# Kernel optimization log

Measured on AMD Instinct MI355X. Metric: run time of the kernel, lower is better.

The kernel has to match this reference:

```python
import jax, jax.numpy as jnp
import numpy as np
from jax import lax

B_, L_, D_MODEL = 2, 1024, 1024
D_STATE, RANK, EXPAND, HEADDIM = 64, 4, 2, 64
D_INNER = EXPAND * D_MODEL
NHEADS = D_INNER // HEADDIM          # 32, divisible by RANK
KCONV = 4
DFF = 4 * D_MODEL
D_PROJ = 2 * D_INNER + 2 * RANK * D_STATE + NHEADS
EPS = 1e-6


def setup_inputs() -> dict:
    key = jax.random.key(0)
    ks = iter(jax.random.split(key, 40))
    def nrm(shape, scale=0.02):
        return jax.random.normal(next(ks), shape, jnp.float32) * scale
    inp = {
        "x": jax.random.normal(next(ks), (B_, L_, D_MODEL), jnp.float32),
        "mask": jnp.ones((B_, L_), jnp.bool_),
        "norm1_w": jnp.ones((D_MODEL,), jnp.float32),
        "norm2_w": jnp.ones((D_MODEL,), jnp.float32),
        "gate_w": nrm((D_MODEL, 2 * D_MODEL)),
        "outp_w": nrm((D_MODEL, D_MODEL)),
        "ffn_w1": nrm((DFF, D_MODEL)),
        "ffn_w3": nrm((DFF, D_MODEL)),
        "ffn_w2": nrm((D_MODEL, DFF)),
    }
    for p in ("f", "b"):
        inp[p + "_in_w"] = nrm((D_PROJ, D_MODEL))
        inp[p + "_conv_w"] = nrm((D_INNER, KCONV), 0.2)
        inp[p + "_conv_b"] = jnp.zeros((D_INNER,), jnp.float32)
        inp[p + "_dt_bias"] = nrm((NHEADS,), 0.5)
        inp[p + "_A_log"] = jnp.log(jnp.linspace(1.0, 16.0, NHEADS)).astype(jnp.float32)
        inp[p + "_D"] = jnp.ones((NHEADS,), jnp.float32)
        inp[p + "_out_w"] = nrm((D_MODEL, D_INNER))
    return inp


def rmsnorm(x, w):
    return x * lax.rsqrt(jnp.mean(x * x, axis=-1, keepdims=True) + EPS) * w


def flip_by_mask(x, mask):
    # reverse valid positions along seq dim, keep padding at end
    L = x.shape[1]
    lengths = mask.astype(jnp.int32).sum(axis=1)          # (B,)
    ar = jnp.arange(L, dtype=jnp.int32)[None, :]
    rev = jnp.clip(lengths[:, None] - 1 - ar, 0, L - 1)   # (B,L)
    out = jnp.take_along_axis(x, rev[..., None], axis=1)
    return out * mask[..., None].astype(x.dtype)


def dwconv_causal(x, w, b):
    # x: (B,L,C), w: (C,K) depthwise, causal
    k = w.shape[-1]
    xp = jnp.pad(x, ((0, 0), (k - 1, 0), (0, 0)))
    kern = w.T[:, None, :]                                # (K,1,C) WIO
    y = lax.conv_general_dilated(xp, kern, (1,), 'VALID',
                                 dimension_numbers=('NWC', 'WIO', 'NWC'),
                                 feature_group_count=x.shape[-1])
    return y + b


def ssd_scan(a, Bh, Ch, dt, x4):
    # a,dt:(B,L,H)  Bh,Ch:(B,L,H,N)  x4:(B,L,H,P)
    def step(S, t):
        a_t, B_t, C_t, dt_t, x_t = t
        S = a_t[..., None, None] * S + (dt_t[..., None] * B_t)[..., None] * x_t[..., None, :]
        y = jnp.einsum('bhn,bhnp->bhp', C_t, S)
        return S, y
    S0 = jnp.zeros((a.shape[0], a.shape[2], Bh.shape[-1], x4.shape[-1]), x4.dtype)
    seq = tuple(jnp.moveaxis(t, 1, 0) for t in (a, Bh, Ch, dt, x4))
    _, ys = lax.scan(step, S0, seq)
    return jnp.moveaxis(ys, 0, 1)                          # (B,L,H,P)


def mamba3(h, maskf, in_w, conv_w, conv_b, dt_bias, A_log, D):
    B, L, _ = h.shape
    proj = h @ in_w.T                                      # (B,L,D_PROJ)
    s0, s1, s2, s3 = D_INNER, 2 * D_INNER, 2 * D_INNER + RANK * D_STATE, 2 * D_INNER + 2 * RANK * D_STATE
    z, xs, Bm, Cm, dt = (proj[..., :s0], proj[..., s0:s1], proj[..., s1:s2],
                          proj[..., s2:s3], proj[..., s3:])
    xs = jax.nn.silu(dwconv_causal(xs * maskf[..., None], conv_w, conv_b)) * maskf[..., None]
    dt = jax.nn.softplus(dt + dt_bias) * maskf[..., None]  # (B,L,H)
    A = -jnp.exp(A_log)                                    # (H,)
    a = jnp.exp(dt * A)
    g = NHEADS // RANK
    Bh = jnp.repeat(Bm.reshape(B, L, RANK, D_STATE), g, axis=2)  # (B,L,H,N)
    Ch = jnp.repeat(Cm.reshape(B, L, RANK, D_STATE), g, axis=2)
    x4 = xs.reshape(B, L, NHEADS, HEADDIM)
    y = ssd_scan(a, Bh, Ch, dt, x4) + D[None, None, :, None] * x4
    return y.reshape(B, L, D_INNER) * jax.nn.silu(z)


def reference(x, mask, norm1_w,
              f_in_w, f_conv_w, f_conv_b, f_dt_bias, f_A_log, f_D, f_out_w,
              b_in_w, b_conv_w, b_conv_b, b_dt_bias, b_A_log, b_D, b_out_w,
              gate_w, outp_w, norm2_w, ffn_w1, ffn_w3, ffn_w2):
    maskf = mask.astype(x.dtype)
    h = rmsnorm(x, norm1_w)
    y_f = mamba3(h, maskf, f_in_w, f_conv_w, f_conv_b, f_dt_bias, f_A_log, f_D) @ f_out_w.T
    h_rev = flip_by_mask(h, mask)
    y_b = mamba3(h_rev, maskf, b_in_w, b_conv_w, b_conv_b, b_dt_bias, b_A_log, b_D) @ b_out_w.T
    y_b = flip_by_mask(y_b, mask)
    gate = jax.nn.sigmoid(jnp.concatenate([y_f, y_b], axis=-1) @ gate_w.T)
    x = x + (gate * y_f + (1.0 - gate) * y_b) @ outp_w.T
    h2 = rmsnorm(x, norm2_w)
    x = x + (jax.nn.silu(h2 @ ffn_w1.T) * (h2 @ ffn_w3.T)) @ ffn_w2.T
    return x * maskf[..., None]
```

## Files before the change

### kernel.cpp

```cpp
#include <hip/hip_runtime.h>


#define T_TOK  2048
#define LSEQ   1024
#define DMODEL 1024
#define DINNER 2048
#define DPROJ  4640
#define NHEADS 32
#define DFF    4096
#define QCH    64
#define NCH    16
#define SST    72

using f32x4  = __attribute__((ext_vector_type(4))) float;
using bf16x8 = __attribute__((ext_vector_type(8))) short;

typedef __attribute__((address_space(1))) const void* gas1;
typedef __attribute__((address_space(3))) void* las3;

__device__ __forceinline__ void gld16(const void* g, void* l) {
  __builtin_amdgcn_global_load_lds((gas1)g, (las3)l, 16, 0, 0);
}

#define VMWAIT8() asm volatile("s_waitcnt vmcnt(8)" ::: "memory")
#define VMWAIT4() asm volatile("s_waitcnt vmcnt(4)" ::: "memory")
#define VMWAIT0() asm volatile("s_waitcnt vmcnt(0)" ::: "memory")
#define SCHEDB()  __builtin_amdgcn_sched_barrier(0)
#define BARRIER() __builtin_amdgcn_s_barrier()

__device__ __forceinline__ unsigned short f2bf(float x) {
  unsigned int u = __float_as_uint(x);
  u = (u + 0x7FFFu + ((u >> 16) & 1u)) >> 16;
  return (unsigned short)u;
}
__device__ __forceinline__ float bf2f(unsigned short u) {
  return __uint_as_float((unsigned int)u << 16);
}
__device__ __forceinline__ float siluf_(float x) { return x / (1.f + expf(-x)); }

__device__ __forceinline__ uint4 pack8(const float4& a, const float4& b) {
  uint4 o;
  o.x = (unsigned)f2bf(a.x) | ((unsigned)f2bf(a.y) << 16);
  o.y = (unsigned)f2bf(a.z) | ((unsigned)f2bf(a.w) << 16);
  o.z = (unsigned)f2bf(b.x) | ((unsigned)f2bf(b.y) << 16);
  o.w = (unsigned)f2bf(b.z) | ((unsigned)f2bf(b.w) << 16);
  return o;
}

__device__ __forceinline__ void tile_decode(int& tm, int& tn) {
  const int gx = gridDim.x;
  int flat = blockIdx.y * gx + blockIdx.x;
  int nwg = gx * gridDim.y;
  int cpx = nwg >> 3;
  int swz = (flat & 7) * cpx + (flat >> 3);
  int width = gx << 4;
  int group = swz / width;
  int rem = swz - group * width;
  tm = (group << 4) + (rem & 15);
  tn = rem >> 4;
}

__global__ __launch_bounds__(256) void k_cvt(const float* __restrict__ s,
                                             unsigned short* __restrict__ d, int n) {
  int i = (blockIdx.x * 256 + threadIdx.x) * 4;
  if (i >= n) return;
  float4 v = *(const float4*)(s + i);
  ushort4 o;
  o.x = f2bf(v.x); o.y = f2bf(v.y); o.z = f2bf(v.z); o.w = f2bf(v.w);
  *(ushort4*)(d + i) = o;
}

__global__ __launch_bounds__(256) void k_cvt13(const float* __restrict__ f1,
                                               const float* __restrict__ f3,
                                               unsigned short* __restrict__ d) {
  int i = (blockIdx.x * 256 + threadIdx.x) * 4;
  int R = i >> 10, k = i & 1023;
  const float* src = (R & 1) ? f3 : f1;
  float4 v = *(const float4*)(src + (size_t)(R >> 1) * 1024 + k);
  ushort4 o;
  o.x = f2bf(v.x); o.y = f2bf(v.y); o.z = f2bf(v.z); o.w = f2bf(v.w);
  *(ushort4*)(d + i) = o;
}

__global__ __launch_bounds__(256) void k_rms1(const float* __restrict__ x,
                                              const float* __restrict__ w,
                                              unsigned short* __restrict__ h,
                                              unsigned short* __restrict__ hrev) {
  int row = blockIdx.x;
  int tid = threadIdx.x;
  const float4* xr = (const float4*)(x + (size_t)row * DMODEL);
  float4 v = xr[tid];
  float s = v.x * v.x + v.y * v.y + v.z * v.z + v.w * v.w;
  #pragma unroll
  for (int off = 32; off >= 1; off >>= 1) s += __shfl_down(s, off);
  __shared__ float red[4];
  int lane = tid & 63, wv = tid >> 6;
  if (lane == 0) red[wv] = s;
  __syncthreads();
  float tot = red[0] + red[1] + red[2] + red[3];
  float scale = rsqrtf(tot * (1.0f / 1024.0f) + 1e-6f);
  float4 w4 = ((const float4*)w)[tid];
  ushort4 o;
  o.x = f2bf(v.x * scale * w4.x);
  o.y = f2bf(v.y * scale * w4.y);
  o.z = f2bf(v.z * scale * w4.z);
  o.w = f2bf(v.w * scale * w4.w);
  ((ushort4*)(h + (size_t)row * DMODEL))[tid] = o;
  ((ushort4*)(hrev + (size_t)(row ^ 1023) * DMODEL))[tid] = o;
}

template<int EPI>
__global__ __launch_bounds__(256, 2)
void k_gemmT(const unsigned short* __restrict__ A0, const unsigned short* __restrict__ B0,
             void* __restrict__ C0v,
             const unsigned short* __restrict__ A1, const unsigned short* __restrict__ B1,
             void* __restrict__ C1v, int N, int K, int ldc) {
  __shared__ unsigned short lA0[128 * 64], lB0[128 * 64];
  __shared__ unsigned short lA1[128 * 64], lB1[128 * 64];
  const unsigned short* A = blockIdx.z ? A1 : A0;
  const unsigned short* B = blockIdx.z ? B1 : B0;
  void* Cv = blockIdx.z ? C1v : C0v;

  int tm, tn;
  tile_decode(tm, tn);

  const int tid  = threadIdx.x;
  const int lane = tid & 63;
  const int wave = tid >> 6;
  const int wm = (wave >> 1) * 64, wn = (wave & 1) * 64;
  const int fr = lane & 15, kh = lane >> 4;
  const int sr = lane >> 3;
  const int sc = ((lane & 7) ^ sr) * 8;

  f32x4 acc[4][4];
  #pragma unroll
  for (int m = 0; m < 4; ++m)
    #pragma unroll
    for (int n = 0; n < 4; ++n)
      acc[m][n] = f32x4{0.f, 0.f, 0.f, 0.f};

  auto stage = [&](unsigned short* dA, unsigned short* dB, int kt) {
    #pragma unroll
    for (int i = 0; i < 4; ++i) {
      int r = wave * 32 + i * 8 + sr;
      size_t arow = (size_t)(tm * 128 + r);
      int brow = tn * 128 + r; if (brow > N - 1) brow = N - 1;
      gld16(A + arow * K + kt + sc, dA + (wave * 32 + i * 8) * 64);
      gld16(B + (size_t)brow * K + kt + sc, dB + (wave * 32 + i * 8) * 64);
    }
  };
  auto compute = [&](const unsigned short* sA, const unsigned short* sB) {
    #pragma unroll
    for (int kk = 0; kk < 2; ++kk) {
      bf16x8 af[4], bfv[4];
      #pragma unroll
      for (int m = 0; m < 4; ++m) {
        int row = wm + m * 16 + fr;
        af[m] = *(const bf16x8*)&sA[row * 64 + (((kk * 4 + kh) ^ (row & 7)) * 8)];
      }
      #pragma unroll
      for (int n = 0; n < 4; ++n) {
        int row = wn + n * 16 + fr;
        bfv[n] = *(const bf16x8*)&sB[row * 64 + (((kk * 4 + kh) ^ (row & 7)) * 8)];
      }
      #pragma unroll
      for (int m = 0; m < 4; ++m)
        #pragma unroll
        for (int n = 0; n < 4; ++n)
          acc[m][n] = __builtin_amdgcn_mfma_f32_16x16x32_bf16(af[m], bfv[n], acc[m][n], 0, 0, 0);
    }
  };

  const int nt = K >> 6;
  stage(lA0, lB0, 0);
  for (int t = 0; t < nt; t += 2) {
    if (t + 1 < nt) { stage(lA1, lB1, (t + 1) << 6); VMWAIT8(); } else VMWAIT0();
    SCHEDB(); BARRIER(); SCHEDB();
    compute(lA0, lB0);
    BARRIER(); SCHEDB();
    if (t + 1 < nt) {
      if (t + 2 < nt) { stage(lA0, lB0, (t + 2) << 6); VMWAIT8(); } else VMWAIT0();
      SCHEDB(); BARRIER(); SCHEDB();
      compute(lA1, lB1);
      BARRIER(); SCHEDB();
    }
  }

  #pragma unroll
  for (int m = 0; m < 4; ++m) {
    int grow0 = tm * 128 + wm + m * 16 + kh * 4;
    #pragma unroll
    for (int n = 0; n < 4; ++n) {
      int gcol = tn * 128 + wn + n * 16 + fr;
      if (gcol >= N) continue;
      #pragma unroll
      for (int j = 0; j < 4; ++j) {
        int row = grow0 + j;
        float val = acc[m][n][j];
        if constexpr (EPI == 0) {
          ((float*)Cv)[(size_t)row * ldc + gcol] = val;
        } else {
          float other = __shfl_xor(val, 1);
          if (!(fr & 1))
            ((unsigned short*)Cv)[(size_t)row * DFF + (gcol >> 1)] = f2bf(siluf_(val) * other);
        }
      }
    }
  }
}

template<int EPI>
__global__ __launch_bounds__(256, 4)
void k_gemm64T(const unsigned short* __restrict__ A0, const unsigned short* __restrict__ B0,
               void* __restrict__ C0v,
               const unsigned short* __restrict__ A1, const unsigned short* __restrict__ B1,
               void* __restrict__ C1v, int N, int K, int ldc) {
  __shared__ unsigned short lA0[64 * 64], lB0[64 * 64];
  __shared__ unsigned short lA1[64 * 64], lB1[64 * 64];
  const unsigned short* A = blockIdx.z ? A1 : A0;
  const unsigned short* B = blockIdx.z ? B1 : B0;
  void* Cv = blockIdx.z ? C1v : C0v;

  int tm, tn;
  tile_decode(tm, tn);

  const int tid  = threadIdx.x;
  const int lane = tid & 63;
  const int wave = tid >> 6;
  const int wm = (wave >> 1) * 32, wn = (wave & 1) * 32;
  const int fr = lane & 15, kh = lane >> 4;
  const int sr = lane >> 3;
  const int sc = ((lane & 7) ^ sr) * 8;

  f32x4 acc[2][2];
  #pragma unroll
  for (int m = 0; m < 2; ++m)
    #pragma unroll
    for (int n = 0; n < 2; ++n)
      acc[m][n] = f32x4{0.f, 0.f, 0.f, 0.f};

  auto stage = [&](unsigned short* dA, unsigned short* dB, int kt) {
    #pragma unroll
    for (int i = 0; i < 2; ++i) {
      int r = wave * 16 + i * 8 + sr;
      size_t arow = (size_t)(tm * 64 + r);
      size_t brow = (size_t)(tn * 64 + r);
      gld16(A + arow * K + kt + sc, dA + (wave * 16 + i * 8) * 64);
      gld16(B + brow * K + kt + sc, dB + (wave * 16 + i * 8) * 64);
    }
  };
  auto compute = [&](const unsigned short* sA, const unsigned short* sB) {
    #pragma unroll
    for (int kk = 0; kk < 2; ++kk) {
      bf16x8 af[2], bfv[2];
      #pragma unroll
      for (int m = 0; m < 2; ++m) {
        int row = wm + m * 16 + fr;
        af[m] = *(const bf16x8*)&sA[row * 64 + (((kk * 4 + kh) ^ (row & 7)) * 8)];
      }
      #pragma unroll
      for (int n = 0; n < 2; ++n) {
        int row = wn + n * 16 + fr;
        bfv[n] = *(const bf16x8*)&sB[row * 64 + (((kk * 4 + kh) ^ (row & 7)) * 8)];
      }
      #pragma unroll
      for (int m = 0; m < 2; ++m)
        #pragma unroll
        for (int n = 0; n < 2; ++n)
          acc[m][n] = __builtin_amdgcn_mfma_f32_16x16x32_bf16(af[m], bfv[n], acc[m][n], 0, 0, 0);
    }
  };

  const int nt = K >> 6;
  stage(lA0, lB0, 0);
  for (int t = 0; t < nt; t += 2) {
    if (t + 1 < nt) { stage(lA1, lB1, (t + 1) << 6); VMWAIT4(); } else VMWAIT0();
    SCHEDB(); BARRIER(); SCHEDB();
    compute(lA0, lB0);
    BARRIER(); SCHEDB();
    if (t + 1 < nt) {
      if (t + 2 < nt) { stage(lA0, lB0, (t + 2) << 6); VMWAIT4(); } else VMWAIT0();
      SCHEDB(); BARRIER(); SCHEDB();
      compute(lA1, lB1);
      BARRIER(); SCHEDB();
    }
  }

  #pragma unroll
  for (int m = 0; m < 2; ++m) {
    int grow0 = tm * 64 + wm + m * 16 + kh * 4;
    #pragma unroll
    for (int n = 0; n < 2; ++n) {
      int gcol = tn * 64 + wn + n * 16 + fr;
      #pragma unroll
      for (int j = 0; j < 4; ++j) {
        int row = grow0 + j;
        float val = acc[m][n][j];
        if constexpr (EPI == 0) {
          ((float*)Cv)[(size_t)row * ldc + gcol] = val;
        } else if constexpr (EPI == 1) {
          unsigned short* yc = (unsigned short*)Cv;
          if (blockIdx.z == 0)
            yc[(size_t)row * DINNER + gcol] = f2bf(val);
          else
            yc[(size_t)(row ^ 1023) * DINNER + 1024 + gcol] = f2bf(val);
        } else if constexpr (EPI == 3) {
          float* o = (float*)Cv + (size_t)row * ldc + gcol;
          *o += val;
        } else {
          const unsigned short* yc = (const unsigned short*)C1v;
          float gv = 1.f / (1.f + expf(-val));
          float yf = bf2f(yc[(size_t)row * DINNER + gcol]);
          float yb = bf2f(yc[(size_t)row * DINNER + 1024 + gcol]);
          ((unsigned short*)Cv)[(size_t)row * 1024 + gcol] = f2bf(gv * yf + (1.f - gv) * yb);
        }
      }
    }
  }
}

__global__ __launch_bounds__(256) void k_prep(
    const float* __restrict__ proj, const float* __restrict__ convw,
    const float* __restrict__ convb, const float* __restrict__ dtb,
    const float* __restrict__ Alog,
    float* __restrict__ xs, float* __restrict__ dts, float* __restrict__ las_) {
  int row = blockIdx.x;
  int t = row & 1023;
  int tid = threadIdx.x;
  int c0 = tid * 8;
  float acc[8];
  #pragma unroll
  for (int j = 0; j < 8; ++j) acc[j] = convb[c0 + j];
  #pragma unroll
  for (int tap = 0; tap < 4; ++tap) {
    int tt = t - 3 + tap;
    if (tt < 0) continue;
    const float* src = proj + (size_t)(row - 3 + tap) * DPROJ + 2048 + c0;
    #pragma unroll
    for (int j = 0; j < 8; ++j)
      acc[j] = fmaf(src[j], convw[(c0 + j) * 4 + tap], acc[j]);
  }
  float* dst = xs + (size_t)row * DINNER + c0;
  #pragma unroll
  for (int j = 0; j < 8; ++j) dst[j] = siluf_(acc[j]);

  if (tid < 32) {
    float d = proj[(size_t)row * DPROJ + 4608 + tid] + dtb[tid];
    d = fmaxf(d, 0.f) + log1pf(expf(-fabsf(d)));
    dts[row * 32 + tid] = d;
    las_[row * 32 + tid] = -expf(Alog[tid]) * d;
  }
}

__global__ __launch_bounds__(256) void k_scan1(
    const float* __restrict__ projF, const float* __restrict__ projB,
    const float* __restrict__ xsF, const float* __restrict__ xsB,
    const float* __restrict__ dtF, const float* __restrict__ dtB_,
    const float* __restrict__ laF, const float* __restrict__ laB,
    float* __restrict__ Ssum, float* __restrict__ Pk) {
  const int dir = blockIdx.y;
  const float* proj = dir ? projB : projF;
  const float* xs   = dir ? xsB  : xsF;
  const float* dts  = dir ? dtB_ : dtF;
  const float* las  = dir ? laB  : laF;
  const int job = blockIdx.x;
  const int k = job & 15, h = (job >> 4) & 31, b = job >> 9;
  const int rg = h >> 3;
  const int jid = (dir * 64 + b * 32 + h) * NCH + k;
  const int tid = threadIdx.x;
  const int lane = tid & 63, wave = tid >> 6;
  const int fr = lane & 15, kh = lane >> 4;
  const size_t rb = (size_t)b * LSEQ + k * QCH;

  __shared__ __align__(16) unsigned short sBt[64 * SST];
  __shared__ __align__(16) unsigned short sXw[64 * SST];
  __shared__ float sDt[64], sLa[64], sW[64];

  if (tid < 64) {
    sDt[tid] = dts[(rb + tid) * 32 + h];
    sLa[tid] = las[(rb + tid) * 32 + h];
  }
  __syncthreads();
  if (wave == 0) {
    float v = sLa[lane];
    #pragma unroll
    for (int o = 1; o < 64; o <<= 1) {
      float u = __shfl_up(v, o);
      if (lane >= o) v += u;
    }
    float tot = __shfl(v, 63);
    sW[lane] = sDt[lane] * expf(tot - v);
    if (lane == 0) Pk[jid] = expf(tot);
  }
  __syncthreads();

  {
    int t = tid >> 2, c0 = (tid & 3) * 16;
    float wt = sW[t];
    const float* pB = proj + (rb + t) * DPROJ + 4096 + rg * 64 + c0;
    const float* pX = xs + (rb + t) * DINNER + h * 64 + c0;
    #pragma unroll
    for (int q = 0; q < 4; ++q) {
      float4 bv = *(const float4*)(pB + 4 * q);
      float4 xv = *(const float4*)(pX + 4 * q);
      int c = c0 + 4 * q;
      sBt[(c + 0) * SST + t] = f2bf(bv.x);
      sBt[(c + 1) * SST + t] = f2bf(bv.y);
      sBt[(c + 2) * SST + t] = f2bf(bv.z);
      sBt[(c + 3) * SST + t] = f2bf(bv.w);
      sXw[(c + 0) * SST + t] = f2bf(xv.x * wt);
      sXw[(c + 1) * SST + t] = f2bf(xv.y * wt);
      sXw[(c + 2) * SST + t] = f2bf(xv.z * wt);
      sXw[(c + 3) * SST + t] = f2bf(xv.w * wt);
    }
  }
  __syncthreads();

  f32x4 acc[4];
  #pragma unroll
  for (int n = 0; n < 4; ++n) acc[n] = f32x4{0.f, 0.f, 0.f, 0.f};
  #pragma unroll
  for (int kk = 0; kk < 2; ++kk) {
    int kc = kk * 4 + kh;
    bf16x8 a = *(const bf16x8*)&sXw[(wave * 16 + fr) * SST + kc * 8];
    #pragma unroll
    for (int n = 0; n < 4; ++n) {
      bf16x8 bb = *(const bf16x8*)&sBt[(n * 16 + fr) * SST + kc * 8];
      acc[n] = __builtin_amdgcn_mfma_f32_16x16x32_bf16(a, bb, acc[n], 0, 0, 0);
    }
  }
  float* dst = Ssum + (size_t)jid * 4096;
  #pragma unroll
  for (int n = 0; n < 4; ++n)
    #pragma unroll
    for (int j = 0; j < 4; ++j)
      dst[(wave * 16 + kh * 4 + j) * 64 + n * 16 + fr] = acc[n][j];
}

__global__ __launch_bounds__(256) void k_scan2(float* __restrict__ Sbuf,
                                               const float* __restrict__ Pk) {
  int e = blockIdx.x * 256 + threadIdx.x;
  int dbh = e >> 12, pn = e & 4095;
  float s = 0.f;
  #pragma unroll
  for (int k = 0; k < NCH; ++k) {
    size_t idx = (size_t)(dbh * NCH + k) * 4096 + pn;
    float loc = Sbuf[idx];
    Sbuf[idx] = s;
    s = Pk[dbh * NCH + k] * s + loc;
  }
}

__global__ __launch_bounds__(256) void k_scan3(
    const float* __restrict__ projF, const float* __restrict__ projB,
    const float* __restrict__ xsF, const float* __restrict__ xsB,
    const float* __restrict__ dtF, const float* __restrict__ dtB_,
    const float* __restrict__ laF, const float* __restrict__ laB,
    const float* __restrict__ DF, const float* __restrict__ DB,
    const float* __restrict__ Sstart,
    unsigned short* __restrict__ yzF, unsigned short* __restrict__ yzB) {
  const int dir = blockIdx.y;
  const float* proj = dir ? projB : projF;
  const float* xs   = dir ? xsB  : xsF;
  const float* dts  = dir ? dtB_ : dtF;
  const float* las  = dir ? laB  : laF;
  const float* Dv   = dir ? DB   : DF;
  unsigned short* yzout = dir ? yzB : yzF;

  const int job = blockIdx.x;
  const int k = job & 15, h = (job >> 4) & 31, b = job >> 9;
  const int rg = h >> 3;
  const int jid = (dir * 64 + b * 32 + h) * NCH + k;
  const int tid = threadIdx.x;
  const int lane = tid & 63, wave = tid >> 6;
  const int fr = lane & 15, kh = lane >> 4;
  const float Dh = Dv[h];
  const size_t rb = (size_t)b * LSEQ + k * QCH;

  __shared__ __align__(16) unsigned short sCm[64 * SST];
  __shared__ __align__(16) unsigned short sBm[64 * SST];
  __shared__ __align__(16) unsigned short sXt[64 * SST];
  __shared__ __align__(16) unsigned short sS0[64 * SST];
  __shared__ __align__(16) unsigned short sMm[64 * SST];
  __shared__ float sDt[64], sLa[64], sLc[64];

  if (tid < 64) {
    sDt[tid] = dts[(rb + tid) * 32 + h];
    sLa[tid] = las[(rb + tid) * 32 + h];
  }
  {
    int t = tid >> 2, c0 = (tid & 3) * 16;
    const float* pB = proj + (rb + t) * DPROJ + 4096 + rg * 64 + c0;
    const float* pC = proj + (rb + t) * DPROJ + 4352 + rg * 64 + c0;
    const float* pX = xs + (rb + t) * DINNER + h * 64 + c0;
    const float* pS = Sstart + (size_t)jid * 4096 + t * 64 + c0;
    float4 b0 = *(const float4*)(pB + 0),  b1 = *(const float4*)(pB + 4);
    float4 b2 = *(const float4*)(pB + 8),  b3 = *(const float4*)(pB + 12);
    float4 c0v = *(const float4*)(pC + 0), c1v = *(const float4*)(pC + 4);
    float4 c2v = *(const float4*)(pC + 8), c3v = *(const float4*)(pC + 12);
    float4 s0v = *(const float4*)(pS + 0), s1v = *(const float4*)(pS + 4);
    float4 s2v = *(const float4*)(pS + 8), s3v = *(const float4*)(pS + 12);
    *(uint4*)&sBm[t * SST + c0]     = pack8(b0, b1);
    *(uint4*)&sBm[t * SST + c0 + 8] = pack8(b2, b3);
    *(uint4*)&sCm[t * SST + c0]     = pack8(c0v, c1v);
    *(uint4*)&sCm[t * SST + c0 + 8] = pack8(c2v, c3v);
    *(uint4*)&sS0[t * SST + c0]     = pack8(s0v, s1v);
    *(uint4*)&sS0[t * SST + c0 + 8] = pack8(s2v, s3v);
    #pragma unroll
    for (int q = 0; q < 4; ++q) {
      float4 xv = *(const float4*)(pX + 4 * q);
      int c = c0 + 4 * q;
      sXt[(c + 0) * SST + t] = f2bf(xv.x);
      sXt[(c + 1) * SST + t] = f2bf(xv.y);
      sXt[(c + 2) * SST + t] = f2bf(xv.z);
      sXt[(c + 3) * SST + t] = f2bf(xv.w);
    }
  }
  __syncthreads();
  if (wave == 0) {
    float v = sLa[lane];
    #pragma unroll
    for (int o = 1; o < 64; o <<= 1) {
      float u = __shfl_up(v, o);
      if (lane >= o) v += u;
    }
    sLc[lane] = v;
  }
  __syncthreads();

  f32x4 g[4];
  #pragma unroll
  for (int n = 0; n < 4; ++n) g[n] = f32x4{0.f, 0.f, 0.f, 0.f};
  #pragma unroll
  for (int kk = 0; kk < 2; ++kk) {
    int kc = kk * 4 + kh;
    bf16x8 a = *(const bf16x8*)&sCm[(wave * 16 + fr) * SST + kc * 8];
    #pragma unroll
    for (int n = 0; n < 4; ++n) {
      bf16x8 bb = *(const bf16x8*)&sBm[(n * 16 + fr) * SST + kc * 8];
      g[n] = __builtin_amdgcn_mfma_f32_16x16x32_bf16(a, bb, g[n], 0, 0, 0);
    }
  }
  int t0 = wave * 16 + kh * 4;
  float lct[4];
  #pragma unroll
  for (int j = 0; j < 4; ++j) lct[j] = sLc[t0 + j];
  #pragma unroll
  for (int n = 0; n < 4; ++n) {
    int s = n * 16 + fr;
    float lcs = sLc[s], dtsv = sDt[s];
    #pragma unroll
    for (int j = 0; j < 4; ++j) {
      float m = (s <= t0 + j) ? g[n][j] * expf(lct[j] - lcs) * dtsv : 0.f;
      sMm[(t0 + j) * SST + s] = f2bf(m);
    }
  }
  __syncthreads();

  f32x4 y1[4], y2[4];
  #pragma unroll
  for (int n = 0; n < 4; ++n) { y1[n] = f32x4{0.f,0.f,0.f,0.f}; y2[n] = f32x4{0.f,0.f,0.f,0.f}; }
  #pragma unroll
  for (int kk = 0; kk < 2; ++kk) {
    int kc = kk * 4 + kh;
    bf16x8 am = *(const bf16x8*)&sMm[(wave * 16 + fr) * SST + kc * 8];
    bf16x8 ac = *(const bf16x8*)&sCm[(wave * 16 + fr) * SST + kc * 8];
    #pragma unroll
    for (int n = 0; n < 4; ++n) {
      bf16x8 bx = *(const bf16x8*)&sXt[(n * 16 + fr) * SST + kc * 8];
      bf16x8 bs = *(const bf16x8*)&sS0[(n * 16 + fr) * SST + kc * 8];
      y1[n] = __builtin_amdgcn_mfma_f32_16x16x32_bf16(am, bx, y1[n], 0, 0, 0);
      y2[n] = __builtin_amdgcn_mfma_f32_16x16x32_bf16(ac, bs, y2[n], 0, 0, 0);
    }
  }

  float e[4];
  #pragma unroll
  for (int j = 0; j < 4; ++j) e[j] = expf(lct[j]);
  #pragma unroll
  for (int n = 0; n < 4; ++n) {
    int p = n * 16 + fr;
    #pragma unroll
    for (int j = 0; j < 4; ++j) {
      int t = t0 + j;
      float xv = bf2f(sXt[p * SST + t]);
      float yv = y1[n][j] + e[j] * y2[n][j] + Dh * xv;
      float zv = proj[(rb + t) * DPROJ + h * 64 + p];
      yzout[(rb + t) * DINNER + h * 64 + p] = f2bf(yv * siluf_(zv));
    }
  }
}

__global__ __launch_bounds__(256) void k_resid(const float* __restrict__ x,
                                               const float* __restrict__ delta,
                                               const float* __restrict__ w,
                                               float* __restrict__ xmid,
                                               unsigned short* __restrict__ h2) {
  int row = blockIdx.x;
  int tid = threadIdx.x;
  float4 v = ((const float4*)(x + (size_t)row * DMODEL))[tid];
  float4 d = ((const float4*)(delta + (size_t)row * DMODEL))[tid];
  v.x += d.x; v.y += d.y; v.z += d.z; v.w += d.w;
  ((float4*)(xmid + (size_t)row * DMODEL))[tid] = v;
  float s = v.x * v.x + v.y * v.y + v.z * v.z + v.w * v.w;
  #pragma unroll
  for (int off = 32; off >= 1; off >>= 1) s += __shfl_down(s, off);
  __shared__ float red[4];
  int lane = tid & 63, wv = tid >> 6;
  if (lane == 0) red[wv] = s;
  __syncthreads();
  float tot = red[0] + red[1] + red[2] + red[3];
  float scale = rsqrtf(tot * (1.0f / 1024.0f) + 1e-6f);
  float4 w4 = ((const float4*)w)[tid];
  ushort4 o;
  o.x = f2bf(v.x * scale * w4.x);
  o.y = f2bf(v.y * scale * w4.y);
  o.z = f2bf(v.z * scale * w4.z);
  o.w = f2bf(v.w * scale * w4.w);
  ((ushort4*)(h2 + (size_t)row * DMODEL))[tid] = o;
}

extern "C" void kernel_launch(void* const* d_in, const int* in_sizes, int n_in,
                              void* d_out, int out_size, void* d_ws, size_t ws_size,
                              hipStream_t stream) {
  const float* X     = (const float*)d_in[0];
  const float* N1W   = (const float*)d_in[2];
  const float* N2W   = (const float*)d_in[3];
  const float* GATEW = (const float*)d_in[4];
  const float* OUTPW = (const float*)d_in[5];
  const float* FFN1  = (const float*)d_in[6];
  const float* FFN3  = (const float*)d_in[7];
  const float* FFN2  = (const float*)d_in[8];
  const float* IN_W[2]  = {(const float*)d_in[9],  (const float*)d_in[16]};
  const float* CONVW[2] = {(const float*)d_in[10], (const float*)d_in[17]};
  const float* CONVB[2] = {(const float*)d_in[11], (const float*)d_in[18]};
  const float* DTB[2]   = {(const float*)d_in[12], (const float*)d_in[19]};
  const float* ALOG[2]  = {(const float*)d_in[13], (const float*)d_in[20]};
  const float* DVEC[2]  = {(const float*)d_in[14], (const float*)d_in[21]};
  const float* OUT_W[2] = {(const float*)d_in[15], (const float*)d_in[22]};
  float* OUT = (float*)d_out;

  char* ws = (char*)d_ws;
  size_t off = 0;
  auto alloc = [&](size_t b) -> char* {
    char* p = ws + off;
    off += (b + 255) & ~(size_t)255;
    return p;
  };

  unsigned short* w_in[2];
  w_in[0] = (unsigned short*)alloc((size_t)DPROJ * DMODEL * 2);
  w_in[1] = (unsigned short*)alloc((size_t)DPROJ * DMODEL * 2);
  unsigned short* w_out[2];
  w_out[0] = (unsigned short*)alloc((size_t)DMODEL * DINNER * 2);
  w_out[1] = (unsigned short*)alloc((size_t)DMODEL * DINNER * 2);
  unsigned short* w_gate = (unsigned short*)alloc((size_t)DMODEL * DINNER * 2);
  unsigned short* w_outp = (unsigned short*)alloc((size_t)DMODEL * DMODEL * 2);
  unsigned short* w_ffn13 = (unsigned short*)alloc((size_t)2 * DFF * DMODEL * 2);
  unsigned short* w_ffn2 = (unsigned short*)alloc((size_t)DMODEL * DFF * 2);

  unsigned short* h_bf    = (unsigned short*)alloc((size_t)T_TOK * DMODEL * 2);
  unsigned short* hrev_bf = (unsigned short*)alloc((size_t)T_TOK * DMODEL * 2);
  float* proj[2];
  proj[0] = (float*)alloc((size_t)T_TOK * DPROJ * 4);
  proj[1] = (float*)alloc((size_t)T_TOK * DPROJ * 4);
  float* xsb[2];
  xsb[0] = (float*)alloc((size_t)T_TOK * DINNER * 4);
  xsb[1] = (float*)alloc((size_t)T_TOK * DINNER * 4);
  float* dts[2];
  dts[0] = (float*)alloc((size_t)T_TOK * 32 * 4);
  dts[1] = (float*)alloc((size_t)T_TOK * 32 * 4);
  float* las[2];
  las[0] = (float*)alloc((size_t)T_TOK * 32 * 4);
  las[1] = (float*)alloc((size_t)T_TOK * 32 * 4);
  unsigned short* yz[2];
  yz[0] = (unsigned short*)alloc((size_t)T_TOK * DINNER * 2);
  yz[1] = (unsigned short*)alloc((size_t)T_TOK * DINNER * 2);
  char* scanRegion = alloc((size_t)2048 * 4096 * 4);
  unsigned short* comb = (unsigned short*)alloc((size_t)T_TOK * DMODEL * 2);
  unsigned short* h2_bf = (unsigned short*)alloc((size_t)T_TOK * DMODEL * 2);

  float* Sbuf = (float*)scanRegion;
  float* Pkb  = (float*)comb;
  unsigned short* ycat = (unsigned short*)scanRegion;
  float* delta = (float*)(scanRegion + 8388608);
  unsigned short* wglu = (unsigned short*)xsb[0];

  dim3 B256(256);
  auto cvt = [&](const float* s, unsigned short* d, int n) {
    k_cvt<<<dim3((n + 1023) / 1024), B256, 0, stream>>>(s, d, n);
  };
  cvt(IN_W[0], w_in[0], DPROJ * DMODEL);
  cvt(IN_W[1], w_in[1], DPROJ * DMODEL);
  cvt(OUT_W[0], w_out[0], DMODEL * DINNER);
  cvt(OUT_W[1], w_out[1], DMODEL * DINNER);
  cvt(GATEW, w_gate, DMODEL * DINNER);
  cvt(OUTPW, w_outp, DMODEL * DMODEL);
  k_cvt13<<<dim3(2 * DFF * DMODEL / 1024), B256, 0, stream>>>(FFN1, FFN3, w_ffn13);
  cvt(FFN2, w_ffn2, DMODEL * DFF);

  k_rms1<<<dim3(T_TOK), B256, 0, stream>>>(X, N1W, h_bf, hrev_bf);

  k_gemmT<0><<<dim3(37, 16, 2), B256, 0, stream>>>(
      h_bf, w_in[0], (void*)proj[0], hrev_bf, w_in[1], (void*)proj[1],
      DPROJ, DMODEL, DPROJ);

  for (int d = 0; d < 2; ++d)
    k_prep<<<dim3(T_TOK), B256, 0, stream>>>(proj[d], CONVW[d], CONVB[d], DTB[d],
                                             ALOG[d], xsb[d], dts[d], las[d]);

  k_scan1<<<dim3(1024, 2), B256, 0, stream>>>(proj[0], proj[1], xsb[0], xsb[1],
                                              dts[0], dts[1], las[0], las[1],
                                              Sbuf, Pkb);
  k_scan2<<<dim3(2048), B256, 0, stream>>>(Sbuf, Pkb);
  k_scan3<<<dim3(1024, 2), B256, 0, stream>>>(proj[0], proj[1], xsb[0], xsb[1],
                                              dts[0], dts[1], las[0], las[1],
                                              DVEC[0], DVEC[1],
                                              Sbuf, yz[0], yz[1]);

  k_gemm64T<1><<<dim3(16, 32, 2), B256, 0, stream>>>(
      yz[0], w_out[0], (void*)ycat, yz[1], w_out[1], (void*)ycat,
      DMODEL, DINNER, DMODEL);

  k_gemm64T<4><<<dim3(16, 32, 1), B256, 0, stream>>>(
      ycat, w_gate, (void*)comb, ycat, w_gate, (void*)ycat, DMODEL, DINNER, 1024);
  k_gemm64T<0><<<dim3(16, 32, 1), B256, 0, stream>>>(
      comb, w_outp, (void*)delta, comb, w_outp, (void*)delta, DMODEL, DMODEL, DMODEL);

  k_resid<<<dim3(T_TOK), B256, 0, stream>>>(X, delta, N2W, OUT, h2_bf);

  k_gemmT<2><<<dim3(64, 16, 1), B256, 0, stream>>>(
      h2_bf, w_ffn13, (void*)wglu, h2_bf, w_ffn13, (void*)wglu, 2 * DFF, DMODEL, 0);
  k_gemm64T<3><<<dim3(16, 32, 1), B256, 0, stream>>>(
      wglu, w_ffn2, (void*)OUT, wglu, w_ffn2, (void*)OUT, DMODEL, DFF, DMODEL);
}
```

Measured before the change: 397.1 us.

## Store projection and conv activations in bf16 and simplify the 128-tile GEMM loop

The input-projection GEMM now writes its output in bf16 instead of fp32, and the conv/SiLU output xs is also stored as bf16. The prep and scan kernels read bf16 directly, with some staging becoming plain copies. This roughly halves the memory traffic of the largest intermediate buffers. In the same change the 128x128 GEMM drops its double-buffered LDS pipeline for a single buffer with __syncthreads, and raises occupancy to 3 blocks per unit, which risks exposing load latency in the in-projection and FFN GEMMs. It also adds precision risk from rounding dt and z inputs to bf16, and reuses scratch space for the GLU buffer.

```diff
diff --git a/kernel.cpp b/kernel.cpp
--- a/kernel.cpp
+++ b/kernel.cpp
@@ -22,7 +22,6 @@
   __builtin_amdgcn_global_load_lds((gas1)g, (las3)l, 16, 0, 0);
 }
 
-#define VMWAIT8() asm volatile("s_waitcnt vmcnt(8)" ::: "memory")
 #define VMWAIT4() asm volatile("s_waitcnt vmcnt(4)" ::: "memory")
 #define VMWAIT0() asm volatile("s_waitcnt vmcnt(0)" ::: "memory")
 #define SCHEDB()  __builtin_amdgcn_sched_barrier(0)
@@ -38,12 +37,12 @@
 }
 __device__ __forceinline__ float siluf_(float x) { return x / (1.f + expf(-x)); }
 
-__device__ __forceinline__ uint4 pack8(const float4& a, const float4& b) {
+__device__ __forceinline__ uint4 pack8f(const float* v) {
   uint4 o;
-  o.x = (unsigned)f2bf(a.x) | ((unsigned)f2bf(a.y) << 16);
-  o.y = (unsigned)f2bf(a.z) | ((unsigned)f2bf(a.w) << 16);
-  o.z = (unsigned)f2bf(b.x) | ((unsigned)f2bf(b.y) << 16);
-  o.w = (unsigned)f2bf(b.z) | ((unsigned)f2bf(b.w) << 16);
+  o.x = (unsigned)f2bf(v[0]) | ((unsigned)f2bf(v[1]) << 16);
+  o.y = (unsigned)f2bf(v[2]) | ((unsigned)f2bf(v[3]) << 16);
+  o.z = (unsigned)f2bf(v[4]) | ((unsigned)f2bf(v[5]) << 16);
+  o.w = (unsigned)f2bf(v[6]) | ((unsigned)f2bf(v[7]) << 16);
   return o;
 }
 
@@ -110,13 +109,12 @@
 }
 
 template<int EPI>
-__global__ __launch_bounds__(256, 2)
+__global__ __launch_bounds__(256, 3)
 void k_gemmT(const unsigned short* __restrict__ A0, const unsigned short* __restrict__ B0,
              void* __restrict__ C0v,
              const unsigned short* __restrict__ A1, const unsigned short* __restrict__ B1,
              void* __restrict__ C1v, int N, int K, int ldc) {
-  __shared__ unsigned short lA0[128 * 64], lB0[128 * 64];
-  __shared__ unsigned short lA1[128 * 64], lB1[128 * 64];
+  __shared__ unsigned short lA[128 * 64], lB[128 * 64];
   const unsigned short* A = blockIdx.z ? A1 : A0;
   const unsigned short* B = blockIdx.z ? B1 : B0;
   void* Cv = blockIdx.z ? C1v : C0v;
@@ -139,29 +137,28 @@
     for (int n = 0; n < 4; ++n)
       acc[m][n] = f32x4{0.f, 0.f, 0.f, 0.f};
 
-  auto stage = [&](unsigned short* dA, unsigned short* dB, int kt) {
+  for (int kt = 0; kt < K; kt += 64) {
     #pragma unroll
     for (int i = 0; i < 4; ++i) {
       int r = wave * 32 + i * 8 + sr;
       size_t arow = (size_t)(tm * 128 + r);
       int brow = tn * 128 + r; if (brow > N - 1) brow = N - 1;
-      gld16(A + arow * K + kt + sc, dA + (wave * 32 + i * 8) * 64);
-      gld16(B + (size_t)brow * K + kt + sc, dB + (wave * 32 + i * 8) * 64);
-    }
-  };
-  auto compute = [&](const unsigned short* sA, const unsigned short* sB) {
+      gld16(A + arow * K + kt + sc, lA + (wave * 32 + i * 8) * 64);
+      gld16(B + (size_t)brow * K + kt + sc, lB + (wave * 32 + i * 8) * 64);
+    }
+    __syncthreads();
     #pragma unroll
     for (int kk = 0; kk < 2; ++kk) {
       bf16x8 af[4], bfv[4];
       #pragma unroll
       for (int m = 0; m < 4; ++m) {
         int row = wm + m * 16 + fr;
-        af[m] = *(const bf16x8*)&sA[row * 64 + (((kk * 4 + kh) ^ (row & 7)) * 8)];
+        af[m] = *(const bf16x8*)&lA[row * 64 + (((kk * 4 + kh) ^ (row & 7)) * 8)];
       }
       #pragma unroll
       for (int n = 0; n < 4; ++n) {
         int row = wn + n * 16 + fr;
-        bfv[n] = *(const bf16x8*)&sB[row * 64 + (((kk * 4 + kh) ^ (row & 7)) * 8)];
+        bfv[n] = *(const bf16x8*)&lB[row * 64 + (((kk * 4 + kh) ^ (row & 7)) * 8)];
       }
       #pragma unroll
       for (int m = 0; m < 4; ++m)
@@ -169,21 +166,7 @@
         for (int n = 0; n < 4; ++n)
           acc[m][n] = __builtin_amdgcn_mfma_f32_16x16x32_bf16(af[m], bfv[n], acc[m][n], 0, 0, 0);
     }
-  };
-
-  const int nt = K >> 6;
-  stage(lA0, lB0, 0);
-  for (int t = 0; t < nt; t += 2) {
-    if (t + 1 < nt) { stage(lA1, lB1, (t + 1) << 6); VMWAIT8(); } else VMWAIT0();
-    SCHEDB(); BARRIER(); SCHEDB();
-    compute(lA0, lB0);
-    BARRIER(); SCHEDB();
-    if (t + 1 < nt) {
-      if (t + 2 < nt) { stage(lA0, lB0, (t + 2) << 6); VMWAIT8(); } else VMWAIT0();
-      SCHEDB(); BARRIER(); SCHEDB();
-      compute(lA1, lB1);
-      BARRIER(); SCHEDB();
-    }
+    __syncthreads();
   }
 
   #pragma unroll
@@ -197,8 +180,8 @@
       for (int j = 0; j < 4; ++j) {
         int row = grow0 + j;
         float val = acc[m][n][j];
-        if constexpr (EPI == 0) {
-          ((float*)Cv)[(size_t)row * ldc + gcol] = val;
+        if constexpr (EPI == 5) {
+          ((unsigned short*)Cv)[(size_t)row * ldc + gcol] = f2bf(val);
         } else {
           float other = __shfl_xor(val, 1);
           if (!(fr & 1))
@@ -320,10 +303,10 @@
 }
 
 __global__ __launch_bounds__(256) void k_prep(
-    const float* __restrict__ proj, const float* __restrict__ convw,
+    const unsigned short* __restrict__ proj, const float* __restrict__ convw,
     const float* __restrict__ convb, const float* __restrict__ dtb,
     const float* __restrict__ Alog,
-    float* __restrict__ xs, float* __restrict__ dts, float* __restrict__ las_) {
+    unsigned short* __restrict__ xs, float* __restrict__ dts, float* __restrict__ las_) {
   int row = blockIdx.x;
   int t = row & 1023;
   int tid = threadIdx.x;
@@ -335,17 +318,18 @@
   for (int tap = 0; tap < 4; ++tap) {
     int tt = t - 3 + tap;
     if (tt < 0) continue;
-    const float* src = proj + (size_t)(row - 3 + tap) * DPROJ + 2048 + c0;
+    const unsigned short* src = proj + (size_t)(row - 3 + tap) * DPROJ + 2048 + c0;
     #pragma unroll
     for (int j = 0; j < 8; ++j)
-      acc[j] = fmaf(src[j], convw[(c0 + j) * 4 + tap], acc[j]);
-  }
-  float* dst = xs + (size_t)row * DINNER + c0;
-  #pragma unroll
-  for (int j = 0; j < 8; ++j) dst[j] = siluf_(acc[j]);
+      acc[j] = fmaf(bf2f(src[j]), convw[(c0 + j) * 4 + tap], acc[j]);
+  }
+  float o[8];
+  #pragma unroll
+  for (int j = 0; j < 8; ++j) o[j] = siluf_(acc[j]);
+  *(uint4*)(xs + (size_t)row * DINNER + c0) = pack8f(o);
 
   if (tid < 32) {
-    float d = proj[(size_t)row * DPROJ + 4608 + tid] + dtb[tid];
+    float d = bf2f(proj[(size_t)row * DPROJ + 4608 + tid]) + dtb[tid];
     d = fmaxf(d, 0.f) + log1pf(expf(-fabsf(d)));
     dts[row * 32 + tid] = d;
     las_[row * 32 + tid] = -expf(Alog[tid]) * d;
@@ -353,14 +337,14 @@
 }
 
 __global__ __launch_bounds__(256) void k_scan1(
-    const float* __restrict__ projF, const float* __restrict__ projB,
-    const float* __restrict__ xsF, const float* __restrict__ xsB,
+    const unsigned short* __restrict__ projF, const unsigned short* __restrict__ projB,
+    const unsigned short* __restrict__ xsF, const unsigned short* __restrict__ xsB,
     const float* __restrict__ dtF, const float* __restrict__ dtB_,
     const float* __restrict__ laF, const float* __restrict__ laB,
     float* __restrict__ Ssum, float* __restrict__ Pk) {
   const int dir = blockIdx.y;
-  const float* proj = dir ? projB : projF;
-  const float* xs   = dir ? xsB  : xsF;
+  const unsigned short* proj = dir ? projB : projF;
+  const unsigned short* xs   = dir ? xsB  : xsF;
   const float* dts  = dir ? dtB_ : dtF;
   const float* las  = dir ? laB  : laF;
   const int job = blockIdx.x;
@@ -397,21 +381,12 @@
   {
     int t = tid >> 2, c0 = (tid & 3) * 16;
     float wt = sW[t];
-    const float* pB = proj + (rb + t) * DPROJ + 4096 + rg * 64 + c0;
-    const float* pX = xs + (rb + t) * DINNER + h * 64 + c0;
-    #pragma unroll
-    for (int q = 0; q < 4; ++q) {
-      float4 bv = *(const float4*)(pB + 4 * q);
-      float4 xv = *(const float4*)(pX + 4 * q);
-      int c = c0 + 4 * q;
-      sBt[(c + 0) * SST + t] = f2bf(bv.x);
-      sBt[(c + 1) * SST + t] = f2bf(bv.y);
-      sBt[(c + 2) * SST + t] = f2bf(bv.z);
-      sBt[(c + 3) * SST + t] = f2bf(bv.w);
-      sXw[(c + 0) * SST + t] = f2bf(xv.x * wt);
-      sXw[(c + 1) * SST + t] = f2bf(xv.y * wt);
-      sXw[(c + 2) * SST + t] = f2bf(xv.z * wt);
-      sXw[(c + 3) * SST + t] = f2bf(xv.w * wt);
+    const unsigned short* pB = proj + (rb + t) * DPROJ + 4096 + rg * 64 + c0;
+    const unsigned short* pX = xs + (rb + t) * DINNER + h * 64 + c0;
+    #pragma unroll
+    for (int q = 0; q < 16; ++q) {
+      sBt[(c0 + q) * SST + t] = pB[q];
+      sXw[(c0 + q) * SST + t] = f2bf(bf2f(pX[q]) * wt);
     }
   }
   __syncthreads();
@@ -452,16 +427,16 @@
 }
 
 __global__ __launch_bounds__(256) void k_scan3(
-    const float* __restrict__ projF, const float* __restrict__ projB,
-    const float* __restrict__ xsF, const float* __restrict__ xsB,
+    const unsigned short* __restrict__ projF, const unsigned short* __restrict__ projB,
+    const unsigned short* __restrict__ xsF, const unsigned short* __restrict__ xsB,
     const float* __restrict__ dtF, const float* __restrict__ dtB_,
     const float* __restrict__ laF, const float* __restrict__ laB,
     const float* __restrict__ DF, const float* __restrict__ DB,
     const float* __restrict__ Sstart,
     unsigned short* __restrict__ yzF, unsigned short* __restrict__ yzB) {
   const int dir = blockIdx.y;
-  const float* proj = dir ? projB : projF;
-  const float* xs   = dir ? xsB  : xsF;
+  const unsigned short* proj = dir ? projB : projF;
+  const unsigned short* xs   = dir ? xsB  : xsF;
   const float* dts  = dir ? dtB_ : dtF;
   const float* las  = dir ? laB  : laF;
   const float* Dv   = dir ? DB   : DF;
@@ -490,31 +465,21 @@
   }
   {
     int t = tid >> 2, c0 = (tid & 3) * 16;
-    const float* pB = proj + (rb + t) * DPROJ + 4096 + rg * 64 + c0;
-    const float* pC = proj + (rb + t) * DPROJ + 4352 + rg * 64 + c0;
-    const float* pX = xs + (rb + t) * DINNER + h * 64 + c0;
+    const unsigned short* pB = proj + (rb + t) * DPROJ + 4096 + rg * 64 + c0;
+    const unsigned short* pC = proj + (rb + t) * DPROJ + 4352 + rg * 64 + c0;
+    const unsigned short* pX = xs + (rb + t) * DINNER + h * 64 + c0;
     const float* pS = Sstart + (size_t)jid * 4096 + t * 64 + c0;
-    float4 b0 = *(const float4*)(pB + 0),  b1 = *(const float4*)(pB + 4);
-    float4 b2 = *(const float4*)(pB + 8),  b3 = *(const float4*)(pB + 12);
-    float4 c0v = *(const float4*)(pC + 0), c1v = *(const float4*)(pC + 4);
-    float4 c2v = *(const float4*)(pC + 8), c3v = *(const float4*)(pC + 12);
-    float4 s0v = *(const float4*)(pS + 0), s1v = *(const float4*)(pS + 4);
-    float4 s2v = *(const float4*)(pS + 8), s3v = *(const float4*)(pS + 12);
-    *(uint4*)&sBm[t * SST + c0]     = pack8(b0, b1);
-    *(uint4*)&sBm[t * SST + c0 + 8] = pack8(b2, b3);
-    *(uint4*)&sCm[t * SST + c0]     = pack8(c0v, c1v);
-    *(uint4*)&sCm[t * SST + c0 + 8] = pack8(c2v, c3v);
-    *(uint4*)&sS0[t * SST + c0]     = pack8(s0v, s1v);
-    *(uint4*)&sS0[t * SST + c0 + 8] = pack8(s2v, s3v);
-    #pragma unroll
-    for (int q = 0; q < 4; ++q) {
-      float4 xv = *(const float4*)(pX + 4 * q);
-      int c = c0 + 4 * q;
-      sXt[(c + 0) * SST + t] = f2bf(xv.x);
-      sXt[(c + 1) * SST + t] = f2bf(xv.y);
-      sXt[(c + 2) * SST + t] = f2bf(xv.z);
-      sXt[(c + 3) * SST + t] = f2bf(xv.w);
-    }
+    *(uint4*)&sBm[t * SST + c0]     = *(const uint4*)(pB);
+    *(uint4*)&sBm[t * SST + c0 + 8] = *(const uint4*)(pB + 8);
+    *(uint4*)&sCm[t * SST + c0]     = *(const uint4*)(pC);
+    *(uint4*)&sCm[t * SST + c0 + 8] = *(const uint4*)(pC + 8);
+    float sv[16];
+    #pragma unroll
+    for (int q = 0; q < 16; ++q) sv[q] = pS[q];
+    *(uint4*)&sS0[t * SST + c0]     = pack8f(sv);
+    *(uint4*)&sS0[t * SST + c0 + 8] = pack8f(sv + 8);
+    #pragma unroll
+    for (int q = 0; q < 16; ++q) sXt[(c0 + q) * SST + t] = pX[q];
   }
   __syncthreads();
   if (wave == 0) {
@@ -585,7 +550,7 @@
       int t = t0 + j;
       float xv = bf2f(sXt[p * SST + t]);
       float yv = y1[n][j] + e[j] * y2[n][j] + Dh * xv;
-      float zv = proj[(rb + t) * DPROJ + h * 64 + p];
+      float zv = bf2f(proj[(rb + t) * DPROJ + h * 64 + p]);
       yzout[(rb + t) * DINNER + h * 64 + p] = f2bf(yv * siluf_(zv));
     }
   }
@@ -661,12 +626,12 @@
 
   unsigned short* h_bf    = (unsigned short*)alloc((size_t)T_TOK * DMODEL * 2);
   unsigned short* hrev_bf = (unsigned short*)alloc((size_t)T_TOK * DMODEL * 2);
-  float* proj[2];
-  proj[0] = (float*)alloc((size_t)T_TOK * DPROJ * 4);
-  proj[1] = (float*)alloc((size_t)T_TOK * DPROJ * 4);
-  float* xsb[2];
-  xsb[0] = (float*)alloc((size_t)T_TOK * DINNER * 4);
-  xsb[1] = (float*)alloc((size_t)T_TOK * DINNER * 4);
+  unsigned short* proj[2];
+  proj[0] = (unsigned short*)alloc((size_t)T_TOK * DPROJ * 2);
+  proj[1] = (unsigned short*)alloc((size_t)T_TOK * DPROJ * 2);
+  unsigned short* xsb[2];
+  xsb[0] = (unsigned short*)alloc((size_t)T_TOK * DINNER * 2);
+  xsb[1] = (unsigned short*)alloc((size_t)T_TOK * DINNER * 2);
   float* dts[2];
   dts[0] = (float*)alloc((size_t)T_TOK * 32 * 4);
   dts[1] = (float*)alloc((size_t)T_TOK * 32 * 4);
@@ -684,7 +649,7 @@
   float* Pkb  = (float*)comb;
   unsigned short* ycat = (unsigned short*)scanRegion;
   float* delta = (float*)(scanRegion + 8388608);
-  unsigned short* wglu = (unsigned short*)xsb[0];
+  unsigned short* wglu = (unsigned short*)scanRegion;
 
   dim3 B256(256);
   auto cvt = [&](const float* s, unsigned short* d, int n) {
@@ -701,7 +666,7 @@
 
   k_rms1<<<dim3(T_TOK), B256, 0, stream>>>(X, N1W, h_bf, hrev_bf);
 
-  k_gemmT<0><<<dim3(37, 16, 2), B256, 0, stream>>>(
+  k_gemmT<5><<<dim3(37, 16, 2), B256, 0, stream>>>(
       h_bf, w_in[0], (void*)proj[0], hrev_bf, w_in[1], (void*)proj[1],
       DPROJ, DMODEL, DPROJ);
 
```

New measurement: 369.3 us. -7.0%, faster.
